# Optimization experiments

Hardware: AMD Instinct MI355X
Metric: run time of the kernel (lower is better)

## Reference

```python
import jax, jax.numpy as jnp
import numpy as np

NEG_INF = -9e16
SLOPE = 0.2  # leaky relu slope


def setup_inputs() -> dict:
    key = jax.random.key(0)
    k1, k2, k3, k4 = jax.random.split(key, 4)
    N, F_in, H, D = 3072, 512, 8, 64
    h = jax.random.normal(k1, (N, F_in), dtype=jnp.float32)
    adj = jax.random.randint(k2, (N, N), 0, 2, dtype=jnp.int32)
    W = jax.random.normal(k3, (H, F_in, D), dtype=jnp.float32) * (2.0 / (F_in + D)) ** 0.5
    a = jax.random.normal(k4, (H, 2 * D, 1), dtype=jnp.float32) * (2.0 / (2 * D + 1)) ** 0.5
    return {"h": h, "adj": adj, "W": W, "a": a}


def reference(h, adj, W, a):
    # h: [N, F], W: [H, F, D], a: [H, 2D, 1], adj: [N, N]
    H, _, D = W.shape
    ht = jnp.einsum("nf,hfd->hnd", h, W)            # [H, N, D]
    a_src = a[:, :D, 0]                               # [H, D]
    a_dst = a[:, D:, 0]                               # [H, D]
    src = jnp.einsum("hnd,hd->hn", ht, a_src)        # [H, N]
    dst = jnp.einsum("hnd,hd->hn", ht, a_dst)        # [H, N]
    e = src[:, :, None] + dst[:, None, :]             # [H, N, N]
    e = jnp.where(e > 0, e, SLOPE * e)                # leaky relu
    e = jnp.where(adj[None] > 0, e, NEG_INF)
    att = jax.nn.softmax(e, axis=-1)                  # [H, N, N]
    hp = jnp.einsum("hnm,hmd->hnd", att, ht)         # [H, N, D]
    out = jnp.transpose(hp, (1, 0, 2)).reshape(h.shape[0], H * D)  # concat heads
    return (out, att)
```

## Files before the change

kernel.cpp:

```cpp
#include <hip/hip_runtime.h>

#define NN 3072
#define FF 512
#define HH 8
#define DD 64
#define SLOPEV 0.2f
#define CH 128
#define NCH (NN/CH)

typedef __bf16  bf16x8 __attribute__((ext_vector_type(8)));
typedef __bf16  bf16x4 __attribute__((ext_vector_type(4)));
typedef short   s16x8  __attribute__((ext_vector_type(8)));
typedef float   f32x4  __attribute__((ext_vector_type(4)));
typedef unsigned long long u64;

#define MFMA16(a,b,c) __builtin_amdgcn_mfma_f32_16x16x32_bf16((a),(b),(c),0,0,0)

__device__ __forceinline__ short f2bf(float x){ __bf16 b=(__bf16)x; return __builtin_bit_cast(short,b); }
__device__ __forceinline__ float bf2f(short s){ return (float)__builtin_bit_cast(__bf16,s); }
__device__ __forceinline__ bf16x8 ldbf8(const short* p){ return __builtin_bit_cast(bf16x8, *(const s16x8*)p); }

__global__ __launch_bounds__(256) void k_split_h(const float* __restrict__ h,
    short* __restrict__ hhi, short* __restrict__ hlo){
  size_t base = ((size_t)blockIdx.x*256 + threadIdx.x)*8;
  float4 v0 = *(const float4*)(h+base);
  float4 v1 = *(const float4*)(h+base+4);
  float vv[8] = {v0.x,v0.y,v0.z,v0.w,v1.x,v1.y,v1.z,v1.w};
  s16x8 hi, lo;
  #pragma unroll
  for (int j=0;j<8;j++){ short s=f2bf(vv[j]); hi[j]=s; lo[j]=f2bf(vv[j]-bf2f(s)); }
  *(s16x8*)(hhi+base)=hi; *(s16x8*)(hlo+base)=lo;
}

__global__ __launch_bounds__(64) void k_wt(const float* __restrict__ W, const float* __restrict__ a,
    short* __restrict__ wthi, short* __restrict__ wtlo,
    float* __restrict__ wasrc, float* __restrict__ wadst){
  int h = blockIdx.y, f0 = blockIdx.x*8, d = threadIdx.x;
  float asv = a[h*2*DD + d];
  float adv = a[h*2*DD + DD + d];
  s16x8 vh, vl;
  #pragma unroll
  for (int j=0;j<8;j++){
    float v = W[((size_t)h*FF + f0 + j)*DD + d];
    short s = f2bf(v); vh[j]=s; vl[j]=f2bf(v-bf2f(s));
    float ws_ = v*asv, wd_ = v*adv;
    #pragma unroll
    for (int m=1;m<64;m<<=1){ ws_ += __shfl_xor(ws_,m,64); wd_ += __shfl_xor(wd_,m,64); }
    if (d==0){ wasrc[h*FF+f0+j]=ws_; wadst[h*FF+f0+j]=wd_; }
  }
  size_t o = ((size_t)h*DD + d)*FF + f0;
  *(s16x8*)(wthi+o)=vh; *(s16x8*)(wtlo+o)=vl;
}

__global__ __launch_bounds__(256) void k_pack(const int* __restrict__ adj, u64* __restrict__ padj){
  int idx = blockIdx.x*256 + threadIdx.x;
  u64 b = __ballot(adj[idx] > 0);
  if ((threadIdx.x & 63) == 0) padj[idx>>6] = b;
}

__global__ __launch_bounds__(256) void k_srcdst(const float* __restrict__ h,
    const float* __restrict__ wasrc, const float* __restrict__ wadst,
    float* __restrict__ src, float* __restrict__ dst){
  int wid = blockIdx.x*4 + (threadIdx.x>>6);
  int lane = threadIdx.x & 63;
  int hh = wid / NN, n = wid - hh*NN;
  const float* hp = h + (size_t)n*FF + lane*8;
  const float* sp = wasrc + (size_t)hh*FF + lane*8;
  const float* dp = wadst + (size_t)hh*FF + lane*8;
  float4 x0 = *(const float4*)hp, x1 = *(const float4*)(hp+4);
  float4 s0 = *(const float4*)sp, s1 = *(const float4*)(sp+4);
  float4 t0 = *(const float4*)dp, t1 = *(const float4*)(dp+4);
  float s = x0.x*s0.x + x0.y*s0.y + x0.z*s0.z + x0.w*s0.w
          + x1.x*s1.x + x1.y*s1.y + x1.z*s1.z + x1.w*s1.w;
  float t = x0.x*t0.x + x0.y*t0.y + x0.z*t0.z + x0.w*t0.w
          + x1.x*t1.x + x1.y*t1.y + x1.z*t1.z + x1.w*t1.w;
  #pragma unroll
  for (int m=1;m<64;m<<=1){ s += __shfl_xor(s,m,64); t += __shfl_xor(t,m,64); }
  if (lane==0){ src[hh*NN+n]=s; dst[hh*NN+n]=t; }
}

__global__ __launch_bounds__(128) void k_ht(const short* __restrict__ hhi, const short* __restrict__ hlo,
    const short* __restrict__ wthi, const short* __restrict__ wtlo,
    short* __restrict__ hthi, short* __restrict__ htlo){
  int h = blockIdx.y, n0 = blockIdx.x*32;
  int w = threadIdx.x>>6, lane = threadIdx.x&63;
  int r15 = lane&15, g = lane>>4;
  int arow = n0 + w*16 + r15;
  f32x4 acc[4] = {{0.f,0.f,0.f,0.f},{0.f,0.f,0.f,0.f},{0.f,0.f,0.f,0.f},{0.f,0.f,0.f,0.f}};
  const short* ha = hhi + (size_t)arow*FF + g*8;
  const short* la = hlo + (size_t)arow*FF + g*8;
  for (int kk=0; kk<FF; kk+=32){
    bf16x8 ahi = ldbf8(ha+kk), alo = ldbf8(la+kk);
    #pragma unroll
    for (int c=0;c<4;c++){
      size_t bo = ((size_t)h*DD + c*16 + r15)*FF + g*8 + kk;
      bf16x8 bh = ldbf8(wthi + bo), bl = ldbf8(wtlo + bo);
      acc[c] = MFMA16(ahi,bh,acc[c]);
      acc[c] = MFMA16(ahi,bl,acc[c]);
      acc[c] = MFMA16(alo,bh,acc[c]);
    }
  }
  #pragma unroll
  for (int c=0;c<4;c++){
    #pragma unroll
    for (int r=0;r<4;r++){
      float v = acc[c][r];
      short s = f2bf(v); short sl = f2bf(v - bf2f(s));
      int n = n0 + w*16 + g*4 + r;
      size_t o = ((size_t)h*DD + c*16 + r15)*NN + n;
      hthi[o]=s; htlo[o]=sl;
    }
  }
}

__global__ __launch_bounds__(512, 6) void k_att(const u64* __restrict__ padj,
    const float* __restrict__ src, const float* __restrict__ dst,
    const short* __restrict__ hthi, const short* __restrict__ htlo,
    float* __restrict__ dout){
  __shared__ short lhi[64][CH];
  __shared__ short llo[64][CH];
  __shared__ short pt [32][CH];
  const size_t OUTOFF = (size_t)NN*HH*DD;
  int h = blockIdx.y, n0 = blockIdx.x*32;
  int t = threadIdx.x;
  int r = t>>4, j = t&15;
  int nrow = n0 + r;
  float srcv = src[h*NN + nrow];
  const float* dsth = dst + h*NN;
  const u64* arow = padj + (size_t)nrow*(NN/64);

  float psum = 0.f;
  for (int c=0;c<NCH;c++){
    u64 w0 = arow[c*2], w1 = arow[c*2+1];
    const float* dp = dsth + c*CH + j*4;
    float4 d0 = *(const float4*)dp, d1 = *(const float4*)(dp+64);
    float dj[8] = {d0.x,d0.y,d0.z,d0.w,d1.x,d1.y,d1.z,d1.w};
    #pragma unroll
    for (int e=0;e<8;e++){
      float ev = srcv + dj[e];
      ev = fmaxf(ev, SLOPEV*ev);
      u64 bits = (e<4) ? w0 : w1;
      float p = ((bits >> (j*4 + (e&3))) & 1ull) ? __expf(ev) : 0.f;
      psum += p;
    }
  }
  #pragma unroll
  for (int m=1;m<16;m<<=1) psum += __shfl_xor(psum, m, 64);
  float inv = (psum > 0.f) ? 1.f/psum : (1.f/(float)NN);
  bool am = !(psum > 0.f);

  int lane = t&63, r15 = lane&15, g = lane>>4;
  int wv = t>>6, cblk = wv&3, nh = wv>>2;
  f32x4 acc = {0.f,0.f,0.f,0.f};
  float* attrow = dout + OUTOFF + ((size_t)(h*NN + nrow))*NN;
  int sd = t>>4;
  const short* ghi0 = hthi + ((size_t)(h*DD) + sd   )*NN + j*8;
  const short* ghi1 = hthi + ((size_t)(h*DD) + sd+32)*NN + j*8;
  const short* glo0 = htlo + ((size_t)(h*DD) + sd   )*NN + j*8;
  const short* glo1 = htlo + ((size_t)(h*DD) + sd+32)*NN + j*8;
  int swz_w = (j*16) ^ ((sd&7)<<4);
  int pb1o = (j*8)        ^ ((r&7)<<4);
  int pb2o = (128 + j*8)  ^ ((r&7)<<4);
  char* lhB = (char*)&lhi[0][0];
  char* llB = (char*)&llo[0][0];
  char* ptB = (char*)&pt[0][0];

  for (int c=0;c<NCH;c++){
    int m0 = c*CH;
    s16x8 v0 = *(const s16x8*)(ghi0 + m0);
    s16x8 v1 = *(const s16x8*)(ghi1 + m0);
    s16x8 v2 = *(const s16x8*)(glo0 + m0);
    s16x8 v3 = *(const s16x8*)(glo1 + m0);
    u64 w0 = arow[c*2], w1 = arow[c*2+1];
    const float* dp = dsth + m0 + j*4;
    float4 d0 = *(const float4*)dp, d1 = *(const float4*)(dp+64);
    float dj[8] = {d0.x,d0.y,d0.z,d0.w,d1.x,d1.y,d1.z,d1.w};
    float o[8];
    #pragma unroll
    for (int e=0;e<8;e++){
      float ev = srcv + dj[e];
      ev = fmaxf(ev, SLOPEV*ev);
      u64 bits = (e<4) ? w0 : w1;
      float p = ((bits >> (j*4 + (e&3))) & 1ull) ? __expf(ev) : 0.f;
      if (am) p = 1.f;
      o[e] = p * inv;
    }
    f32x4 s0 = {o[0],o[1],o[2],o[3]};
    f32x4 s1 = {o[4],o[5],o[6],o[7]};
    __builtin_nontemporal_store(s0, (f32x4*)(attrow+m0+j*4));
    __builtin_nontemporal_store(s1, (f32x4*)(attrow+m0+64+j*4));
    *(s16x8*)(lhB + sd*(CH*2)     + swz_w) = v0;
    *(s16x8*)(lhB + (sd+32)*(CH*2)+ swz_w) = v1;
    *(s16x8*)(llB + sd*(CH*2)     + swz_w) = v2;
    *(s16x8*)(llB + (sd+32)*(CH*2)+ swz_w) = v3;
    bf16x4 pb0, pb1;
    #pragma unroll
    for (int e=0;e<4;e++){ pb0[e] = (__bf16)o[e]; pb1[e] = (__bf16)o[e+4]; }
    *(bf16x4*)(ptB + r*(CH*2) + pb1o) = pb0;
    *(bf16x4*)(ptB + r*(CH*2) + pb2o) = pb1;
    __syncthreads();
    #pragma unroll
    for (int ks=0;ks<4;ks++){
      int cb = (ks*64 + g*16) ^ ((r15&7)<<4);
      bf16x8 bf = *(const bf16x8*)(ptB + (nh*16+r15)*(CH*2) + cb);
      bf16x8 ah = *(const bf16x8*)(lhB + (cblk*16+r15)*(CH*2) + cb);
      bf16x8 al = *(const bf16x8*)(llB + (cblk*16+r15)*(CH*2) + cb);
      acc = MFMA16(ah, bf, acc);
      acc = MFMA16(al, bf, acc);
    }
    __syncthreads();
  }

  int n = n0 + nh*16 + r15;
  size_t ob = (size_t)n*(HH*DD) + h*DD + cblk*16 + g*4;
  __builtin_nontemporal_store(acc, (f32x4*)(dout+ob));
}

extern "C" void kernel_launch(void* const* d_in, const int* in_sizes, int n_in,
                              void* d_out, int out_size, void* d_ws, size_t ws_size,
                              hipStream_t stream) {
  const float* h   = (const float*)d_in[0];
  const int*   adj = (const int*)d_in[1];
  const float* W   = (const float*)d_in[2];
  const float* a   = (const float*)d_in[3];
  float* out = (float*)d_out;

  short* hhi  = (short*)d_ws;
  short* hlo  = hhi  + (size_t)NN*FF;
  short* wthi = hlo  + (size_t)NN*FF;
  short* wtlo = wthi + (size_t)HH*DD*FF;
  short* hthi = wtlo + (size_t)HH*DD*FF;
  short* htlo = hthi + (size_t)HH*DD*NN;
  float* wasrc= (float*)(htlo + (size_t)HH*DD*NN);
  float* wadst= wasrc + HH*FF;
  float* srcb = wadst + HH*FF;
  float* dstb = srcb + HH*NN;
  u64*   padj = (u64*)(dstb + HH*NN);

  k_split_h<<<dim3(NN*FF/(256*8)), 256, 0, stream>>>(h, hhi, hlo);
  k_wt     <<<dim3(FF/8, HH), 64, 0, stream>>>(W, a, wthi, wtlo, wasrc, wadst);
  k_pack   <<<dim3(NN*NN/256), 256, 0, stream>>>(adj, padj);
  k_srcdst <<<dim3(HH*NN/4), 256, 0, stream>>>(h, wasrc, wadst, srcb, dstb);
  k_ht     <<<dim3(NN/32, HH), 128, 0, stream>>>(hhi, hlo, wthi, wtlo, hthi, htlo);
  k_att    <<<dim3(NN/32, HH), 512, 0, stream>>>(padj, srcb, dstb, hthi, htlo, out);
}
```

Measured before the change: 161.5 us.

## Double-buffer ht tiles via async global-to-LDS loads and fuse per-head src/dst

The attention kernel shrinks its column chunk to 64. It double-buffers the ht hi/lo tiles in shared memory, using global_load_lds asynchronous copies to prefetch the next chunk while the current one is processed. The adjacency bits and dst values are prefetched one iteration ahead, one of the two barriers per iteration becomes a bare s_barrier, the grid is flattened so the eight heads of a row block run adjacently, and occupancy is raised to 8 blocks per SIMD target. The src/dst projection kernel now computes all heads per node so each row of h is loaded once rather than eight times. The aim is to hide global-load latency behind the MFMA and softmax work and to reuse adjacency and h data across heads. The cost is more synchronisation steps and a reliance on the async LDS loads being complete at the barrier.

```diff
diff --git a/kernel.cpp b/kernel.cpp
--- a/kernel.cpp
+++ b/kernel.cpp
@@ -5,8 +5,8 @@
 #define HH 8
 #define DD 64
 #define SLOPEV 0.2f
-#define CH 128
-#define NCH (NN/CH)
+#define CH2 64
+#define NC2 (NN/CH2)
 
 typedef __bf16  bf16x8 __attribute__((ext_vector_type(8)));
 typedef __bf16  bf16x4 __attribute__((ext_vector_type(4)));
@@ -19,6 +19,12 @@
 __device__ __forceinline__ short f2bf(float x){ __bf16 b=(__bf16)x; return __builtin_bit_cast(short,b); }
 __device__ __forceinline__ float bf2f(short s){ return (float)__builtin_bit_cast(__bf16,s); }
 __device__ __forceinline__ bf16x8 ldbf8(const short* p){ return __builtin_bit_cast(bf16x8, *(const s16x8*)p); }
+
+__device__ __forceinline__ void gload16(const void* g, void* l){
+  __builtin_amdgcn_global_load_lds(
+      (const __attribute__((address_space(1))) void*)(uintptr_t)g,
+      (__attribute__((address_space(3))) void*)(uint32_t)(uintptr_t)l, 16, 0, 0);
+}
 
 __global__ __launch_bounds__(256) void k_split_h(const float* __restrict__ h,
     short* __restrict__ hhi, short* __restrict__ hlo){
@@ -61,22 +67,32 @@
 __global__ __launch_bounds__(256) void k_srcdst(const float* __restrict__ h,
     const float* __restrict__ wasrc, const float* __restrict__ wadst,
     float* __restrict__ src, float* __restrict__ dst){
-  int wid = blockIdx.x*4 + (threadIdx.x>>6);
+  int n = blockIdx.x*4 + (threadIdx.x>>6);
   int lane = threadIdx.x & 63;
-  int hh = wid / NN, n = wid - hh*NN;
   const float* hp = h + (size_t)n*FF + lane*8;
-  const float* sp = wasrc + (size_t)hh*FF + lane*8;
-  const float* dp = wadst + (size_t)hh*FF + lane*8;
   float4 x0 = *(const float4*)hp, x1 = *(const float4*)(hp+4);
-  float4 s0 = *(const float4*)sp, s1 = *(const float4*)(sp+4);
-  float4 t0 = *(const float4*)dp, t1 = *(const float4*)(dp+4);
-  float s = x0.x*s0.x + x0.y*s0.y + x0.z*s0.z + x0.w*s0.w
-          + x1.x*s1.x + x1.y*s1.y + x1.z*s1.z + x1.w*s1.w;
-  float t = x0.x*t0.x + x0.y*t0.y + x0.z*t0.z + x0.w*t0.w
-          + x1.x*t1.x + x1.y*t1.y + x1.z*t1.z + x1.w*t1.w;
-  #pragma unroll
-  for (int m=1;m<64;m<<=1){ s += __shfl_xor(s,m,64); t += __shfl_xor(t,m,64); }
-  if (lane==0){ src[hh*NN+n]=s; dst[hh*NN+n]=t; }
+  float xs[8] = {x0.x,x0.y,x0.z,x0.w,x1.x,x1.y,x1.z,x1.w};
+  float ps[HH], pd[HH];
+  #pragma unroll
+  for (int hh=0; hh<HH; hh++){
+    const float* sp = wasrc + (size_t)hh*FF + lane*8;
+    const float* dp = wadst + (size_t)hh*FF + lane*8;
+    float4 s0 = *(const float4*)sp, s1 = *(const float4*)(sp+4);
+    float4 t0 = *(const float4*)dp, t1 = *(const float4*)(dp+4);
+    ps[hh] = xs[0]*s0.x + xs[1]*s0.y + xs[2]*s0.z + xs[3]*s0.w
+           + xs[4]*s1.x + xs[5]*s1.y + xs[6]*s1.z + xs[7]*s1.w;
+    pd[hh] = xs[0]*t0.x + xs[1]*t0.y + xs[2]*t0.z + xs[3]*t0.w
+           + xs[4]*t1.x + xs[5]*t1.y + xs[6]*t1.z + xs[7]*t1.w;
+  }
+  #pragma unroll
+  for (int m=1;m<64;m<<=1){
+    #pragma unroll
+    for (int hh=0; hh<HH; hh++){ ps[hh] += __shfl_xor(ps[hh],m,64); pd[hh] += __shfl_xor(pd[hh],m,64); }
+  }
+  if (lane==0){
+    #pragma unroll
+    for (int hh=0; hh<HH; hh++){ src[hh*NN+n]=ps[hh]; dst[hh*NN+n]=pd[hh]; }
+  }
 }
 
 __global__ __launch_bounds__(128) void k_ht(const short* __restrict__ hhi, const short* __restrict__ hlo,
@@ -113,15 +129,15 @@
   }
 }
 
-__global__ __launch_bounds__(512, 6) void k_att(const u64* __restrict__ padj,
+__global__ __launch_bounds__(512, 8) void k_att(const u64* __restrict__ padj,
     const float* __restrict__ src, const float* __restrict__ dst,
     const short* __restrict__ hthi, const short* __restrict__ htlo,
     float* __restrict__ dout){
-  __shared__ short lhi[64][CH];
-  __shared__ short llo[64][CH];
-  __shared__ short pt [32][CH];
+  __shared__ short hA[64][CH2], lA[64][CH2], hB[64][CH2], lB[64][CH2];
+  __shared__ short pA[32][CH2], pB[32][CH2];
   const size_t OUTOFF = (size_t)NN*HH*DD;
-  int h = blockIdx.y, n0 = blockIdx.x*32;
+  int bid = blockIdx.x;
+  int h = bid & 7, n0 = (bid >> 3) * 32;
   int t = threadIdx.x;
   int r = t>>4, j = t&15;
   int nrow = n0 + r;
@@ -129,10 +145,20 @@
   const float* dsth = dst + h*NN;
   const u64* arow = padj + (size_t)nrow*(NN/64);
 
+  int wv = t>>6, lane = t&63, r15 = lane&15, g = lane>>4;
+  int cblk = wv&3, nh = wv>>2;
+  int drow = t>>3;
+  int sslot = (t&7) ^ (drow&7);
+  const short* gh = hthi + ((size_t)(h*DD) + drow)*NN + sslot*8;
+  const short* gl = htlo + ((size_t)(h*DD) + drow)*NN + sslot*8;
+
+  gload16(gh, &hA[wv*8][0]);
+  gload16(gl, &lA[wv*8][0]);
+
   float psum = 0.f;
-  for (int c=0;c<NCH;c++){
+  for (int c=0;c<24;c++){
     u64 w0 = arow[c*2], w1 = arow[c*2+1];
-    const float* dp = dsth + c*CH + j*4;
+    const float* dp = dsth + c*128 + j*4;
     float4 d0 = *(const float4*)dp, d1 = *(const float4*)(dp+64);
     float dj[8] = {d0.x,d0.y,d0.z,d0.w,d1.x,d1.y,d1.z,d1.w};
     #pragma unroll
@@ -149,66 +175,65 @@
   float inv = (psum > 0.f) ? 1.f/psum : (1.f/(float)NN);
   bool am = !(psum > 0.f);
 
-  int lane = t&63, r15 = lane&15, g = lane>>4;
-  int wv = t>>6, cblk = wv&3, nh = wv>>2;
   f32x4 acc = {0.f,0.f,0.f,0.f};
   float* attrow = dout + OUTOFF + ((size_t)(h*NN + nrow))*NN;
-  int sd = t>>4;
-  const short* ghi0 = hthi + ((size_t)(h*DD) + sd   )*NN + j*8;
-  const short* ghi1 = hthi + ((size_t)(h*DD) + sd+32)*NN + j*8;
-  const short* glo0 = htlo + ((size_t)(h*DD) + sd   )*NN + j*8;
-  const short* glo1 = htlo + ((size_t)(h*DD) + sd+32)*NN + j*8;
-  int swz_w = (j*16) ^ ((sd&7)<<4);
-  int pb1o = (j*8)        ^ ((r&7)<<4);
-  int pb2o = (128 + j*8)  ^ ((r&7)<<4);
-  char* lhB = (char*)&lhi[0][0];
-  char* llB = (char*)&llo[0][0];
-  char* ptB = (char*)&pt[0][0];
-
-  for (int c=0;c<NCH;c++){
-    int m0 = c*CH;
-    s16x8 v0 = *(const s16x8*)(ghi0 + m0);
-    s16x8 v1 = *(const s16x8*)(ghi1 + m0);
-    s16x8 v2 = *(const s16x8*)(glo0 + m0);
-    s16x8 v3 = *(const s16x8*)(glo1 + m0);
-    u64 w0 = arow[c*2], w1 = arow[c*2+1];
-    const float* dp = dsth + m0 + j*4;
-    float4 d0 = *(const float4*)dp, d1 = *(const float4*)(dp+64);
-    float dj[8] = {d0.x,d0.y,d0.z,d0.w,d1.x,d1.y,d1.z,d1.w};
-    float o[8];
-    #pragma unroll
-    for (int e=0;e<8;e++){
-      float ev = srcv + dj[e];
+  int aoff0 = (cblk*16 + r15)*(CH2*2);
+  int boff0 = (nh*16 + r15)*(CH2*2);
+  int csw   = (r15&7)<<4;
+  int pofs  = r*(CH2*2) + ((j*8) ^ ((r&7)<<4));
+
+  u64 bits = arow[0];
+  const float* dvp = dsth + j*4;
+  float4 dv = *(const float4*)dvp;
+
+  #pragma unroll 2
+  for (int c=0;c<NC2;c++){
+    short (*hc)[CH2]; short (*lc)[CH2]; short (*hn)[CH2]; short (*ln)[CH2]; short (*pc)[CH2];
+    if (c&1){ hc=hB; lc=lB; hn=hA; ln=lA; pc=pB; }
+    else    { hc=hA; lc=lA; hn=hB; ln=lB; pc=pA; }
+
+    if (c < NC2-1){
+      gload16(gh + (c+1)*CH2, &hn[wv*8][0]);
+      gload16(gl + (c+1)*CH2, &ln[wv*8][0]);
+    }
+    u64 bits_n = 0; float4 dv_n = {0,0,0,0};
+    if (c < NC2-1){
+      bits_n = arow[c+1];
+      dv_n = *(const float4*)(dvp + (c+1)*CH2);
+    }
+    float o[4];
+    #pragma unroll
+    for (int e=0;e<4;e++){
+      float ev = srcv + ((const float*)&dv)[e];
       ev = fmaxf(ev, SLOPEV*ev);
-      u64 bits = (e<4) ? w0 : w1;
-      float p = ((bits >> (j*4 + (e&3))) & 1ull) ? __expf(ev) : 0.f;
+      float p = ((bits >> (j*4 + e)) & 1ull) ? __expf(ev) : 0.f;
       if (am) p = 1.f;
       o[e] = p * inv;
     }
     f32x4 s0 = {o[0],o[1],o[2],o[3]};
-    f32x4 s1 = {o[4],o[5],o[6],o[7]};
-    __builtin_nontemporal_store(s0, (f32x4*)(attrow+m0+j*4));
-    __builtin_nontemporal_store(s1, (f32x4*)(attrow+m0+64+j*4));
-    *(s16x8*)(lhB + sd*(CH*2)     + swz_w) = v0;
-    *(s16x8*)(lhB + (sd+32)*(CH*2)+ swz_w) = v1;
-    *(s16x8*)(llB + sd*(CH*2)     + swz_w) = v2;
-    *(s16x8*)(llB + (sd+32)*(CH*2)+ swz_w) = v3;
-    bf16x4 pb0, pb1;
-    #pragma unroll
-    for (int e=0;e<4;e++){ pb0[e] = (__bf16)o[e]; pb1[e] = (__bf16)o[e+4]; }
-    *(bf16x4*)(ptB + r*(CH*2) + pb1o) = pb0;
-    *(bf16x4*)(ptB + r*(CH*2) + pb2o) = pb1;
+    __builtin_nontemporal_store(s0, (f32x4*)(attrow + c*CH2 + j*4));
+    bf16x4 pb;
+    #pragma unroll
+    for (int e=0;e<4;e++) pb[e] = (__bf16)o[e];
+    *(bf16x4*)((char*)pc + pofs) = pb;
+
     __syncthreads();
-    #pragma unroll
-    for (int ks=0;ks<4;ks++){
-      int cb = (ks*64 + g*16) ^ ((r15&7)<<4);
-      bf16x8 bf = *(const bf16x8*)(ptB + (nh*16+r15)*(CH*2) + cb);
-      bf16x8 ah = *(const bf16x8*)(lhB + (cblk*16+r15)*(CH*2) + cb);
-      bf16x8 al = *(const bf16x8*)(llB + (cblk*16+r15)*(CH*2) + cb);
+
+    const char* hcB = (const char*)hc;
+    const char* lcB = (const char*)lc;
+    const char* pcB = (const char*)pc;
+    #pragma unroll
+    for (int ks=0;ks<2;ks++){
+      int kb = (g*16 + ks*64) ^ csw;
+      bf16x8 bf = *(const bf16x8*)(pcB + boff0 + kb);
+      bf16x8 ah = *(const bf16x8*)(hcB + aoff0 + kb);
+      bf16x8 al = *(const bf16x8*)(lcB + aoff0 + kb);
       acc = MFMA16(ah, bf, acc);
       acc = MFMA16(al, bf, acc);
     }
-    __syncthreads();
+    __builtin_amdgcn_s_barrier();
+
+    bits = bits_n; dv = dv_n;
   }
 
   int n = n0 + nh*16 + r15;
@@ -240,7 +265,7 @@
   k_split_h<<<dim3(NN*FF/(256*8)), 256, 0, stream>>>(h, hhi, hlo);
   k_wt     <<<dim3(FF/8, HH), 64, 0, stream>>>(W, a, wthi, wtlo, wasrc, wadst);
   k_pack   <<<dim3(NN*NN/256), 256, 0, stream>>>(adj, padj);
-  k_srcdst <<<dim3(HH*NN/4), 256, 0, stream>>>(h, wasrc, wadst, srcb, dstb);
+  k_srcdst <<<dim3(NN/4), 256, 0, stream>>>(h, wasrc, wadst, srcb, dstb);
   k_ht     <<<dim3(NN/32, HH), 128, 0, stream>>>(hhi, hlo, wthi, wtlo, hthi, htlo);
-  k_att    <<<dim3(NN/32, HH), 512, 0, stream>>>(padj, srcb, dstb, hthi, htlo, out);
-}
+  k_att    <<<dim3(NN/32*HH), 512, 0, stream>>>(padj, srcb, dstb, hthi, htlo, out);
+}
```

After: 161.9 us. About the same (+0.3%).
